# Kernel tuning notes

Hardware: AMD Instinct MI355X
Metric: run time of the kernel (lower is better)

Reference implementation:

```python
import jax, jax.numpy as jnp
import numpy as np

DIM = 512
CODEBOOK_SIZE = 8192


def setup_inputs() -> dict:
    key = jax.random.key(0)
    k1, k2 = jax.random.split(key)
    x = jax.random.normal(k1, (8, 1024, DIM), dtype=jnp.float32)
    embed_weight = jax.random.normal(k2, (CODEBOOK_SIZE, DIM), dtype=jnp.float32)
    return {"x": x, "embed_weight": embed_weight}


def reference(x, embed_weight):
    # flatten: [..., d] -> [N, d]
    shape = x.shape
    flatten = x.reshape(-1, shape[-1])                      # [N, d]
    x_sq = jnp.sum(flatten * flatten, axis=1, keepdims=True)        # [N, 1]
    e_sq = jnp.sum(embed_weight * embed_weight, axis=1)[None, :]    # [1, K]
    dist = -(x_sq - 2.0 * jnp.einsum('nd,kd->nk', flatten, embed_weight) + e_sq)
    embed_ind = jnp.argmax(dist, axis=-1)                   # [N]
    embed_ind = embed_ind.reshape(shape[:-1])               # [...,]
    quantize = embed_weight[embed_ind]                      # [..., d]
    return quantize, embed_ind
```

## Files before the change

kernel.cpp:

```cpp
#include <hip/hip_runtime.h>
#include <math.h>

#define DIM      512
#define KC       8192
#define NR       8192
#define BM       128
#define BN       256
#define NT       2
#define CHUNK    (BN*NT)
#define NXB      (KC/CHUNK)
#define KT       (DIM/32)
#define EPS      0.125f
#define MAXW     16384

typedef __attribute__((ext_vector_type(8))) _Float16 f16x8;
typedef __attribute__((ext_vector_type(4))) float f32x4;

#define AS1 __attribute__((address_space(1)))
#define AS3 __attribute__((address_space(3)))

static __device__ __forceinline__ unsigned fkey(float f) {
    unsigned b = __float_as_uint(f);
    return (b & 0x80000000u) ? ~b : (b | 0x80000000u);
}

__global__ void pack_kernel(const float* __restrict__ X, const float* __restrict__ E,
                            _Float16* __restrict__ Xp, _Float16* __restrict__ Ep) {
    const float* src = blockIdx.y ? E : X;
    _Float16* dst = blockIdx.y ? Ep : Xp;
    const int tile = blockIdx.x * 4 + (threadIdx.x >> 6);
    const int lane = threadIdx.x & 63;
    const int rt = tile / KT, kt = tile % KT;
    const int row = rt * 16 + (lane & 15);
    const int k   = kt * 32 + (lane >> 4) * 8;
    const float4* p = reinterpret_cast<const float4*>(src + (size_t)row * DIM + k);
    const float4 a = p[0], b = p[1];
    f16x8 o;
    o[0] = (_Float16)a.x; o[1] = (_Float16)a.y; o[2] = (_Float16)a.z; o[3] = (_Float16)a.w;
    o[4] = (_Float16)b.x; o[5] = (_Float16)b.y; o[6] = (_Float16)b.z; o[7] = (_Float16)b.w;
    *reinterpret_cast<f16x8*>(dst + (size_t)tile * 512 + lane * 8) = o;
}

__global__ void esq_kernel(const float* __restrict__ E, float* __restrict__ e_sq,
                           int* __restrict__ fcount) {
    if (blockIdx.x == 0 && threadIdx.x == 0) *fcount = 0;
    const int wave = threadIdx.x >> 6;
    const int lane = threadIdx.x & 63;
    const int row  = blockIdx.x * 4 + wave;
    const float4* p = reinterpret_cast<const float4*>(E + (size_t)row * DIM) + lane * 2;
    float4 a = p[0], b = p[1];
    float s = a.x * a.x + a.y * a.y + a.z * a.z + a.w * a.w
            + b.x * b.x + b.y * b.y + b.z * b.z + b.w * b.w;
    #pragma unroll
    for (int off = 32; off > 0; off >>= 1) s += __shfl_down(s, off, 64);
    if (lane == 0) e_sq[row] = s;
}

__global__ __launch_bounds__(256, 2)
void vq_mfma_kernel(const _Float16* __restrict__ Xp, const _Float16* __restrict__ Ep,
                    const float* __restrict__ e_sq,
                    float* __restrict__ pbest, float* __restrict__ psec,
                    int* __restrict__ pidx)
{
    __shared__ _Float16 lds[24576];

    const int tid  = threadIdx.x;
    const int lane = tid & 63;
    const int w    = tid >> 6;
    const int wr   = w >> 1;
    const int wc   = w & 1;

    const int bid = blockIdx.x;
    const int xcd = bid & 7, pos = bid >> 3;
    const int cx  = xcd * 2 + (pos >> 6);
    const int ry  = pos & 63;
    const int row0  = ry * BM;
    const int cbase = cx * CHUNK;
    const int rtb  = row0 >> 4;
    const int ctb0 = cbase >> 4;

    float s1[16], s2[16];
    int   i1[16];
    #pragma unroll
    for (int i = 0; i < 16; ++i) { s1[i] = -INFINITY; s2[i] = -INFINITY; i1[i] = 0; }

    for (int nt = 0; nt < NT; ++nt) {
        const int code0 = cbase + nt * BN;
        const int ctb = ctb0 + nt * 16;

        f32x4 acc[4][8];
        #pragma unroll
        for (int m = 0; m < 4; ++m)
            #pragma unroll
            for (int n = 0; n < 8; ++n)
                acc[m][n] = (f32x4){0.f, 0.f, 0.f, 0.f};

        for (int ks = 0; ks < 8; ++ks) {
            const int kt2 = ks * 2;
            #pragma unroll
            for (int i = 0; i < 4; ++i) {
                const int t = w * 4 + i;
                const int rt = t >> 1, ktl = t & 1;
                const _Float16* gp = Xp + (((size_t)(rtb + rt) * KT + kt2 + ktl) << 9) + lane * 8;
                __builtin_amdgcn_global_load_lds(
                    (const AS1 void*)gp, (AS3 void*)(lds + t * 512), 16, 0, 0);
            }
            #pragma unroll
            for (int j = 0; j < 8; ++j) {
                const int b = w * 8 + j;
                const int rt = b >> 1, ktl = b & 1;
                const _Float16* gp = Ep + (((size_t)(ctb + rt) * KT + kt2 + ktl) << 9) + lane * 8;
                __builtin_amdgcn_global_load_lds(
                    (const AS1 void*)gp, (AS3 void*)(lds + 8192 + b * 512), 16, 0, 0);
            }
            __syncthreads();

            #pragma unroll
            for (int kk = 0; kk < 2; ++kk) {
                f16x8 bfrag[8];
                #pragma unroll
                for (int n = 0; n < 8; ++n)
                    bfrag[n] = *reinterpret_cast<const f16x8*>(
                        lds + 8192 + ((wc * 8 + n) * 2 + kk) * 512 + lane * 8);
                #pragma unroll
                for (int m = 0; m < 4; ++m) {
                    const f16x8 afrag = *reinterpret_cast<const f16x8*>(
                        lds + ((wr * 4 + m) * 2 + kk) * 512 + lane * 8);
                    #pragma unroll
                    for (int n = 0; n < 8; ++n)
                        acc[m][n] = __builtin_amdgcn_mfma_f32_16x16x32_f16(
                            afrag, bfrag[n], acc[m][n], 0, 0, 0);
                }
            }
            __syncthreads();
        }

        #pragma unroll
        for (int n = 0; n < 8; ++n) {
            const int code = code0 + wc * 128 + n * 16 + (lane & 15);
            const float esv = e_sq[code];
            #pragma unroll
            for (int m = 0; m < 4; ++m) {
                #pragma unroll
                for (int r = 0; r < 4; ++r) {
                    const float sc = fmaf(2.0f, acc[m][n][r], -esv);
                    const int slot = m * 4 + r;
                    if (sc > s1[slot]) { s2[slot] = s1[slot]; s1[slot] = sc; i1[slot] = code; }
                    else if (sc > s2[slot]) { s2[slot] = sc; }
                    else if (sc == s1[slot]) { s2[slot] = sc; }
                }
            }
        }
    }

    #pragma unroll
    for (int slot = 0; slot < 16; ++slot) {
        #pragma unroll
        for (int mask = 1; mask < 16; mask <<= 1) {
            float t1 = __shfl_xor(s1[slot], mask, 64);
            float t2 = __shfl_xor(s2[slot], mask, 64);
            int   j1 = __shfl_xor(i1[slot], mask, 64);
            if (t1 > s1[slot]) { s2[slot] = fmaxf(s1[slot], t2); s1[slot] = t1; i1[slot] = j1; }
            else if (t1 == s1[slot]) { s2[slot] = fmaxf(s2[slot], fmaxf(t1, t2)); i1[slot] = min(i1[slot], j1); }
            else { s2[slot] = fmaxf(s2[slot], t1); }
        }
    }

    __syncthreads();
    float* reds1 = reinterpret_cast<float*>(&lds[0]);
    float* reds2 = reds1 + BM * 2;
    int*   redi  = reinterpret_cast<int*>(reds2 + BM * 2);

    if ((lane & 15) == 0) {
        #pragma unroll
        for (int m = 0; m < 4; ++m)
            #pragma unroll
            for (int r = 0; r < 4; ++r) {
                const int row = wr * 64 + m * 16 + (lane >> 4) * 4 + r;
                reds1[row * 2 + wc] = s1[m * 4 + r];
                reds2[row * 2 + wc] = s2[m * 4 + r];
                redi [row * 2 + wc] = i1[m * 4 + r];
            }
    }
    __syncthreads();

    if (tid < BM) {
        float a1 = reds1[tid * 2 + 0], a2 = reds2[tid * 2 + 0]; int ai = redi[tid * 2 + 0];
        const float b1 = reds1[tid * 2 + 1], b2 = reds2[tid * 2 + 1]; const int bi = redi[tid * 2 + 1];
        if (b1 > a1)       { a2 = fmaxf(a1, b2); a1 = b1; ai = bi; }
        else if (b1 == a1) { a2 = fmaxf(a2, fmaxf(b1, b2)); ai = min(ai, bi); }
        else               { a2 = fmaxf(a2, b1); }
        const int row = row0 + tid;
        pbest[(size_t)row * NXB + cx] = a1;
        psec [(size_t)row * NXB + cx] = a2;
        pidx [(size_t)row * NXB + cx] = ai;
    }
}

__global__ void reduce_kernel(const float* __restrict__ pbest, const float* __restrict__ psec,
                              const int* __restrict__ pidx,
                              int* __restrict__ final_idx, int* __restrict__ flags,
                              int* __restrict__ fcount, int* __restrict__ wlist,
                              unsigned long long* __restrict__ rkey)
{
    const int row = blockIdx.x * 256 + threadIdx.x;
    float pb[NXB];
    float s1 = -INFINITY, s2 = -INFINITY; int i1 = 0;
    #pragma unroll
    for (int j = 0; j < NXB; ++j) {
        const float t1 = pbest[(size_t)row * NXB + j];
        const float t2 = psec [(size_t)row * NXB + j];
        const int   j1 = pidx [(size_t)row * NXB + j];
        pb[j] = t1;
        if (t1 > s1)       { s2 = fmaxf(s1, t2); s1 = t1; i1 = j1; }
        else if (t1 == s1) { s2 = fmaxf(s2, fmaxf(t1, t2)); i1 = min(i1, j1); }
        else               { s2 = fmaxf(s2, t1); }
    }
    final_idx[row] = i1;
    int fl = 0;
    if (s1 - s2 < EPS) {
        fl = 1;
        rkey[row] = 0ULL;
        #pragma unroll
        for (int j = 0; j < NXB; ++j) {
            if (pb[j] >= s1 - EPS) {
                const int p = atomicAdd(fcount, 1);
                if (p < MAXW) wlist[p] = (row << 4) | j;
            }
        }
    }
    flags[row] = fl;
}

__global__ __launch_bounds__(256)
void rescue_kernel(const float* __restrict__ X, const float* __restrict__ E,
                   const float* __restrict__ e_sq,
                   const int* __restrict__ fcount, const int* __restrict__ wlist,
                   unsigned long long* __restrict__ rkey)
{
    const int nw0 = *fcount;
    const int nw  = nw0 < MAXW ? nw0 : MAXW;
    const int lane = threadIdx.x & 63;
    const int w    = threadIdx.x >> 6;
    __shared__ float rb[4];
    __shared__ int   ri[4];

    for (int e = blockIdx.x; e < nw; e += gridDim.x) {
        const int ent = wlist[e];
        const int row = ent >> 4;
        const int j   = ent & 15;

        const float4* xp = reinterpret_cast<const float4*>(X + (size_t)row * DIM) + lane * 2;
        const float4 x0 = xp[0], x1 = xp[1];

        const int c0 = j * CHUNK + w * (CHUNK / 4);
        float best = -INFINITY; int bi = 0;
        for (int c = c0; c < c0 + CHUNK / 4; ++c) {
            const float4* ep = reinterpret_cast<const float4*>(E + (size_t)c * DIM) + lane * 2;
            const float4 e0 = ep[0], e1 = ep[1];
            float dot = x0.x * e0.x;
            dot = fmaf(x0.y, e0.y, dot);
            dot = fmaf(x0.z, e0.z, dot);
            dot = fmaf(x0.w, e0.w, dot);
            dot = fmaf(x1.x, e1.x, dot);
            dot = fmaf(x1.y, e1.y, dot);
            dot = fmaf(x1.z, e1.z, dot);
            dot = fmaf(x1.w, e1.w, dot);
            #pragma unroll
            for (int mask = 1; mask < 64; mask <<= 1) dot += __shfl_xor(dot, mask, 64);
            const float s = fmaf(2.f, dot, -e_sq[c]);
            if (s > best) { best = s; bi = c; }
        }
        if (lane == 0) { rb[w] = best; ri[w] = bi; }
        __syncthreads();
        if (threadIdx.x == 0) {
            float b = rb[0]; int bbi = ri[0];
            #pragma unroll
            for (int q = 1; q < 4; ++q) {
                if (rb[q] > b || (rb[q] == b && ri[q] < bbi)) { b = rb[q]; bbi = ri[q]; }
            }
            const unsigned long long pk =
                ((unsigned long long)fkey(b) << 32) | (unsigned)(8191 - bbi);
            atomicMax(&rkey[row], pk);
        }
        __syncthreads();
    }
}

__global__ void gather_kernel(const int* __restrict__ final_idx,
                              const int* __restrict__ flags,
                              const unsigned long long* __restrict__ rkey,
                              const float* __restrict__ E,
                              float* __restrict__ out_q, float* __restrict__ out_i)
{
    const int row = blockIdx.x;
    __shared__ int s_bi;
    if (threadIdx.x == 0) {
        int bi;
        if (flags[row]) {
            const unsigned long long pk = rkey[row];
            bi = 8191 - (int)(pk & 0xFFFFFFFFull);
        } else {
            bi = final_idx[row];
        }
        s_bi = bi;
        out_i[row] = (float)bi;
    }
    __syncthreads();
    const int bi = s_bi;
    const float4* src = reinterpret_cast<const float4*>(E + (size_t)bi * DIM);
    float4* dst = reinterpret_cast<float4*>(out_q + (size_t)row * DIM);
    dst[threadIdx.x] = src[threadIdx.x];
}

extern "C" void kernel_launch(void* const* d_in, const int* in_sizes, int n_in,
                              void* d_out, int out_size, void* d_ws, size_t ws_size,
                              hipStream_t stream) {
    const float* X = (const float*)d_in[0];
    const float* E = (const float*)d_in[1];

    float* out_q = (float*)d_out;
    float* out_i = (float*)d_out + (size_t)NR * DIM;

    _Float16* Xp = (_Float16*)d_out;
    _Float16* Ep = Xp + (size_t)NR * DIM;

    unsigned long long* rkey = (unsigned long long*)d_ws;
    float* e_sq      = (float*)(rkey + NR);
    float* pbest     = e_sq + KC;
    float* psec      = pbest + (size_t)NR * NXB;
    int*   pidx      = (int*)(psec + (size_t)NR * NXB);
    int*   final_idx = pidx + (size_t)NR * NXB;
    int*   flags     = final_idx + NR;
    int*   wlist     = flags + NR;
    int*   fcount    = wlist + MAXW;

    hipLaunchKernelGGL(esq_kernel, dim3(KC / 4), dim3(256), 0, stream, E, e_sq, fcount);

    hipLaunchKernelGGL(pack_kernel, dim3(NR * DIM / (16 * 32) / 4, 2), dim3(256), 0, stream,
                       X, E, Xp, Ep);

    hipLaunchKernelGGL(vq_mfma_kernel, dim3(NXB * (NR / BM)), dim3(256), 0, stream,
                       Xp, Ep, e_sq, pbest, psec, pidx);

    hipLaunchKernelGGL(reduce_kernel, dim3(NR / 256), dim3(256), 0, stream,
                       pbest, psec, pidx, final_idx, flags, fcount, wlist, rkey);

    hipLaunchKernelGGL(rescue_kernel, dim3(1024), dim3(256), 0, stream,
                       X, E, e_sq, fcount, wlist, rkey);

    hipLaunchKernelGGL(gather_kernel, dim3(NR), dim3(128), 0, stream,
                       final_idx, flags, rkey, E, out_q, out_i);
}
```

Before: 224.5 us.

## Fuse codebook norm into pack kernel and double code tiles per block

Merges the separate e_sq norm kernel into the fp16 pack kernel, so the codebook is read once and one launch is dropped. The pack kernel now has each thread load a contiguous 32-float row segment and write it into the tiled layout. NT goes from 2 to 4, so each block covers twice as many codes and the grid shrinks to 512 blocks. Block-to-tile mapping is simplified to match, which cuts partial-result traffic but also reduces parallelism and changes XCD locality.

```diff
diff --git a/kernel.cpp b/kernel.cpp
--- a/kernel.cpp
+++ b/kernel.cpp
@@ -6,7 +6,7 @@
 #define NR       8192
 #define BM       128
 #define BN       256
-#define NT       2
+#define NT       4
 #define CHUNK    (BN*NT)
 #define NXB      (KC/CHUNK)
 #define KT       (DIM/32)
@@ -25,35 +25,41 @@
 }
 
 __global__ void pack_kernel(const float* __restrict__ X, const float* __restrict__ E,
-                            _Float16* __restrict__ Xp, _Float16* __restrict__ Ep) {
-    const float* src = blockIdx.y ? E : X;
-    _Float16* dst = blockIdx.y ? Ep : Xp;
-    const int tile = blockIdx.x * 4 + (threadIdx.x >> 6);
-    const int lane = threadIdx.x & 63;
-    const int rt = tile / KT, kt = tile % KT;
-    const int row = rt * 16 + (lane & 15);
-    const int k   = kt * 32 + (lane >> 4) * 8;
-    const float4* p = reinterpret_cast<const float4*>(src + (size_t)row * DIM + k);
-    const float4 a = p[0], b = p[1];
-    f16x8 o;
-    o[0] = (_Float16)a.x; o[1] = (_Float16)a.y; o[2] = (_Float16)a.z; o[3] = (_Float16)a.w;
-    o[4] = (_Float16)b.x; o[5] = (_Float16)b.y; o[6] = (_Float16)b.z; o[7] = (_Float16)b.w;
-    *reinterpret_cast<f16x8*>(dst + (size_t)tile * 512 + lane * 8) = o;
-}
-
-__global__ void esq_kernel(const float* __restrict__ E, float* __restrict__ e_sq,
-                           int* __restrict__ fcount) {
-    if (blockIdx.x == 0 && threadIdx.x == 0) *fcount = 0;
-    const int wave = threadIdx.x >> 6;
-    const int lane = threadIdx.x & 63;
-    const int row  = blockIdx.x * 4 + wave;
-    const float4* p = reinterpret_cast<const float4*>(E + (size_t)row * DIM) + lane * 2;
-    float4 a = p[0], b = p[1];
-    float s = a.x * a.x + a.y * a.y + a.z * a.z + a.w * a.w
-            + b.x * b.x + b.y * b.y + b.z * b.z + b.w * b.w;
-    #pragma unroll
-    for (int off = 32; off > 0; off >>= 1) s += __shfl_down(s, off, 64);
-    if (lane == 0) e_sq[row] = s;
+                            _Float16* __restrict__ Xp, _Float16* __restrict__ Ep,
+                            float* __restrict__ e_sq, int* __restrict__ fcount) {
+    if (blockIdx.x == 0 && blockIdx.y == 0 && threadIdx.x == 0) *fcount = 0;
+    const int isE = blockIdx.y;
+    const float* src = isE ? E : X;
+    _Float16* dst = isE ? Ep : Xp;
+    const int t  = threadIdx.x;
+    const int rl = t >> 4;
+    const int kt = t & 15;
+    const int row = blockIdx.x * 16 + rl;
+
+    float4 v[8];
+    const float4* p = reinterpret_cast<const float4*>(src + (size_t)row * DIM + kt * 32);
+    #pragma unroll
+    for (int q = 0; q < 8; ++q) v[q] = p[q];
+
+    _Float16* d = dst + ((size_t)blockIdx.x * 16 + kt) * 512;
+    #pragma unroll
+    for (int kg = 0; kg < 4; ++kg) {
+        const float* vv = reinterpret_cast<const float*>(&v[kg * 2]);
+        f16x8 o;
+        #pragma unroll
+        for (int j = 0; j < 8; ++j) o[j] = (_Float16)vv[j];
+        *reinterpret_cast<f16x8*>(d + (rl + 16 * kg) * 8) = o;
+    }
+
+    if (isE) {
+        const float* vv = reinterpret_cast<const float*>(v);
+        float s = 0.f;
+        #pragma unroll
+        for (int j = 0; j < 32; ++j) s = fmaf(vv[j], vv[j], s);
+        #pragma unroll
+        for (int mask = 1; mask < 16; mask <<= 1) s += __shfl_xor(s, mask, 64);
+        if (kt == 0) e_sq[row] = s;
+    }
 }
 
 __global__ __launch_bounds__(256, 2)
@@ -71,9 +77,8 @@
     const int wc   = w & 1;
 
     const int bid = blockIdx.x;
-    const int xcd = bid & 7, pos = bid >> 3;
-    const int cx  = xcd * 2 + (pos >> 6);
-    const int ry  = pos & 63;
+    const int cx  = bid & 7;
+    const int ry  = bid >> 3;
     const int row0  = ry * BM;
     const int cbase = cx * CHUNK;
     const int rtb  = row0 >> 4;
@@ -335,10 +340,8 @@
     int*   wlist     = flags + NR;
     int*   fcount    = wlist + MAXW;
 
-    hipLaunchKernelGGL(esq_kernel, dim3(KC / 4), dim3(256), 0, stream, E, e_sq, fcount);
-
-    hipLaunchKernelGGL(pack_kernel, dim3(NR * DIM / (16 * 32) / 4, 2), dim3(256), 0, stream,
-                       X, E, Xp, Ep);
+    hipLaunchKernelGGL(pack_kernel, dim3(NR / 16, 2), dim3(256), 0, stream,
+                       X, E, Xp, Ep, e_sq, fcount);
 
     hipLaunchKernelGGL(vq_mfma_kernel, dim3(NXB * (NR / BM)), dim3(256), 0, stream,
                        Xp, Ep, e_sq, pbest, psec, pidx);
```

New measurement: 268.8 us. 19.7% more time.
